# Optimization experiments

Hardware: AMD Instinct MI355X
Metric: run time of the kernel (lower is better)

## Reference

```python
import jax, jax.numpy as jnp
import numpy as np

NEG_INF = -1e9  # additive mask value for masked softmax


def setup_inputs() -> dict:
    key = jax.random.key(0)
    k1, k2, k3, k4, k5 = jax.random.split(key, 5)
    bz, rv_num, rv_len, in_feat, out_feat = 32, 10, 128, 300, 128
    seq_a = jax.random.normal(k1, (bz, rv_num, rv_len, in_feat), dtype=jnp.float32)
    seq_b = jax.random.normal(k2, (bz, rv_num, rv_len, in_feat), dtype=jnp.float32)
    mask_a = jax.random.randint(k3, (bz, rv_num, rv_len), 0, 2, dtype=jnp.int32)
    mask_b = jax.random.randint(k4, (bz, rv_num, rv_len), 0, 2, dtype=jnp.int32)
    # guarantee at least one valid position per review (avoid fully-masked rows)
    mask_a = mask_a.at[:, :, 0].set(1)
    mask_b = mask_b.at[:, :, 0].set(1)
    # FC transform params (xavier-normal-ish weight, zero bias)
    W = jax.random.normal(k5, (in_feat, out_feat), dtype=jnp.float32) * (2.0 / np.sqrt(in_feat + out_feat))
    b = jnp.zeros((out_feat,), dtype=jnp.float32)
    return {"seq_a": seq_a, "seq_b": seq_b, "mask_a": mask_a, "mask_b": mask_b, "W": W, "b": b}


def _masked_softmax(scores, mask):
    # scores: [N, L], mask: [N, L] in {0,1}
    logits = jnp.where(mask > 0, scores, NEG_INF)
    return jax.nn.softmax(logits, axis=-1)


def reference(seq_a, seq_b, mask_a, mask_b, W, b):
    bz, rv_num, rv_len, _ = seq_a.shape
    hdim = W.shape[1]
    N = bz * rv_num          # flattened batch of reviews
    M = rv_num * rv_len      # all tokens on the other side

    # FC + ReLU feature transform
    ta = jax.nn.relu(jnp.einsum('bnld,dh->bnlh', seq_a, W) + b)
    tb = jax.nn.relu(jnp.einsum('bnld,dh->bnlh', seq_b, W) + b)

    sa = ta.reshape(N, rv_len, hdim)
    sb = tb.reshape(N, rv_len, hdim)
    # expand: each review attends over ALL tokens of the other sequence in its sample
    ea = jnp.broadcast_to(ta.reshape(bz, 1, M, hdim), (bz, rv_num, M, hdim)).reshape(N, M, hdim)
    eb = jnp.broadcast_to(tb.reshape(bz, 1, M, hdim), (bz, rv_num, M, hdim)).reshape(N, M, hdim)

    # DOT interaction (no scale): affinity [N, rv_len, M]
    atob_aff = jnp.einsum('nld,nmd->nlm', sa, eb)
    btoa_aff = jnp.einsum('nld,nmd->nlm', sb, ea)

    # MEAN pooling over the other-sequence axis
    atob_scores = atob_aff.mean(axis=-1)  # [N, rv_len]
    btoa_scores = btoa_aff.mean(axis=-1)

    ma = mask_a.reshape(N, rv_len)
    mb = mask_b.reshape(N, rv_len)
    atob_w = _masked_softmax(atob_scores, ma)
    btoa_w = _masked_softmax(btoa_scores, mb)

    a_out = jnp.einsum('nl,nld->nd', atob_w, sa)
    b_out = jnp.einsum('nl,nld->nd', btoa_w, sb)
    return (a_out, b_out, atob_w, btoa_w)
```

## Files before the change

### kernel.cpp

```cpp
#include <hip/hip_runtime.h>
#include <hip/hip_bf16.h>


#define K_FEAT 300
#define H 128
#define NTOK 40960
#define NREV 320
#define TOK_PER_SAMPLE 1280
#define TM 128
#define BLKS_PER_SAMPLE 10
#define LDA 40
#define NCHUNK 10
#define WCHUNK (2 * H * LDA)

typedef __attribute__((ext_vector_type(8))) short bf16x8;
typedef __attribute__((ext_vector_type(4))) float f32x4;
typedef unsigned short u16;
typedef unsigned int u32;

static __device__ __forceinline__ u16 f2bf(float x) {
    u32 u = __float_as_uint(x);
    return (u16)((u + 0x7fffu + ((u >> 16) & 1u)) >> 16);
}
static __device__ __forceinline__ float bf2f(u16 s) {
    return __uint_as_float(((u32)s) << 16);
}

__global__ void wsplit_kernel(const float* __restrict__ W, u16* __restrict__ Wc)
{
    int i = blockIdx.x * 256 + threadIdx.x;
    if (i >= NCHUNK * WCHUNK) return;
    int c = i / WCHUNK;
    int rem = i - c * WCHUNK;
    int part = rem / (H * LDA);
    int rem2 = rem - part * (H * LDA);
    int h = rem2 / LDA;
    int kk = rem2 - h * LDA;
    int k = c * 32 + kk;
    float w = (kk < 32 && k < K_FEAT) ? W[(size_t)k * H + h] : 0.f;
    u16 hi = f2bf(w);
    Wc[i] = part ? f2bf(w - bf2f(hi)) : hi;
}

__global__ __launch_bounds__(256, 3) void fc_mfma_kernel(
    const float* __restrict__ seq_a, const float* __restrict__ seq_b,
    const u16* __restrict__ Wc, const float* __restrict__ bias,
    float* __restrict__ ta, float* __restrict__ tb,
    float* __restrict__ psum_a, float* __restrict__ psum_b)
{
    __shared__ u16 Ah_s[TM * LDA];
    __shared__ u16 Al_s[TM * LDA];
    __shared__ u16 W_s[WCHUNK];
    __shared__ float bias_s[H];

    int blk = blockIdx.x;
    const float* seq; float* outp; float* psum;
    if (blk < 320) { seq = seq_a; outp = ta; psum = psum_a; }
    else           { seq = seq_b; outp = tb; psum = psum_b; blk -= 320; }

    const int tid = threadIdx.x;
    const int tok0 = blk * TM;
    const int wave = tid >> 6;
    const int lane = tid & 63;
    const int nn = lane & 15;
    const int quad = lane >> 4;

    if (tid < H) bias_s[tid] = bias[tid];

    f32x4 acc[8][2];
#pragma unroll
    for (int m = 0; m < 8; ++m) {
        acc[m][0] = (f32x4){0.f, 0.f, 0.f, 0.f};
        acc[m][1] = (f32x4){0.f, 0.f, 0.f, 0.f};
    }

    for (int c = 0; c < NCHUNK; ++c) {
        __syncthreads();
#pragma unroll
        for (int it = 0; it < 4; ++it) {
            int i = tid + it * 256;
            int t = i >> 3;
            int j = i & 7;
            int kk = c * 32 + 4 * j;
            float4 v = make_float4(0.f, 0.f, 0.f, 0.f);
            if (kk + 4 <= K_FEAT)
                v = *(const float4*)&seq[(size_t)(tok0 + t) * K_FEAT + kk];
            u16 h0 = f2bf(v.x), h1 = f2bf(v.y), h2 = f2bf(v.z), h3 = f2bf(v.w);
            uint2 hp, lp;
            hp.x = (u32)h0 | ((u32)h1 << 16);
            hp.y = (u32)h2 | ((u32)h3 << 16);
            lp.x = (u32)f2bf(v.x - bf2f(h0)) | ((u32)f2bf(v.y - bf2f(h1)) << 16);
            lp.y = (u32)f2bf(v.z - bf2f(h2)) | ((u32)f2bf(v.w - bf2f(h3)) << 16);
            *(uint2*)&Ah_s[t * LDA + 4 * j] = hp;
            *(uint2*)&Al_s[t * LDA + 4 * j] = lp;
        }
        const u16* wsrc = Wc + (size_t)c * WCHUNK;
#pragma unroll
        for (int it = 0; it < 5; ++it) {
            int i = tid + it * 256;
            *(uint4*)&W_s[i * 8] = *(const uint4*)&wsrc[i * 8];
        }
        __syncthreads();

        bf16x8 bh0 = *(const bf16x8*)&W_s[((2 * wave + 0) * 16 + nn) * LDA + quad * 8];
        bf16x8 bl0 = *(const bf16x8*)&W_s[5120 + ((2 * wave + 0) * 16 + nn) * LDA + quad * 8];
        bf16x8 bh1 = *(const bf16x8*)&W_s[((2 * wave + 1) * 16 + nn) * LDA + quad * 8];
        bf16x8 bl1 = *(const bf16x8*)&W_s[5120 + ((2 * wave + 1) * 16 + nn) * LDA + quad * 8];
#pragma unroll
        for (int m = 0; m < 8; ++m) {
            bf16x8 a_hi = *(const bf16x8*)&Ah_s[(m * 16 + nn) * LDA + quad * 8];
            bf16x8 a_lo = *(const bf16x8*)&Al_s[(m * 16 + nn) * LDA + quad * 8];
            acc[m][0] = __builtin_amdgcn_mfma_f32_16x16x32_bf16(a_hi, bh0, acc[m][0], 0, 0, 0);
            acc[m][0] = __builtin_amdgcn_mfma_f32_16x16x32_bf16(a_hi, bl0, acc[m][0], 0, 0, 0);
            acc[m][0] = __builtin_amdgcn_mfma_f32_16x16x32_bf16(a_lo, bh0, acc[m][0], 0, 0, 0);
            acc[m][1] = __builtin_amdgcn_mfma_f32_16x16x32_bf16(a_hi, bh1, acc[m][1], 0, 0, 0);
            acc[m][1] = __builtin_amdgcn_mfma_f32_16x16x32_bf16(a_hi, bl1, acc[m][1], 0, 0, 0);
            acc[m][1] = __builtin_amdgcn_mfma_f32_16x16x32_bf16(a_lo, bh1, acc[m][1], 0, 0, 0);
        }
    }

#pragma unroll
    for (int t2 = 0; t2 < 2; ++t2) {
        int hcol = (2 * wave + t2) * 16 + nn;
        float bv = bias_s[hcol];
        float fs = 0.f;
#pragma unroll
        for (int m = 0; m < 8; ++m) {
#pragma unroll
            for (int reg = 0; reg < 4; ++reg) {
                int tok = tok0 + m * 16 + quad * 4 + reg;
                float v = fmaxf(acc[m][t2][reg] + bv, 0.f);
                outp[(size_t)tok * H + hcol] = v;
                fs += v;
            }
        }
        fs += __shfl_xor(fs, 16);
        fs += __shfl_xor(fs, 32);
        if (quad == 0) psum[(size_t)blk * H + hcol] = fs;
    }
}

__global__ __launch_bounds__(256) void attn_kernel(
    const float* __restrict__ ta, const float* __restrict__ tb,
    const int* __restrict__ mask_a, const int* __restrict__ mask_b,
    const float* __restrict__ psum_a, const float* __restrict__ psum_b,
    float* __restrict__ out)
{
    int n = blockIdx.x;
    int side = 0;
    if (n >= NREV) { side = 1; n -= NREV; }

    const float* t = side ? tb : ta;
    const int* mask = side ? mask_b : mask_a;
    const float* psum_o = side ? psum_a : psum_b;
    float* out_vec = out + (side ? NREV * H : 0);
    float* out_w = out + 2 * NREV * H + (side ? NREV * H : 0);

    int sample = n / 10;
    int tid = threadIdx.x;

    __shared__ float score_part[128 * 33];
    __shared__ float mean_s[128];
    __shared__ float w_s[128];
    __shared__ float red[4];
    __shared__ float part_out[8 * 128];

    if (tid < 128) {
        float s = 0.f;
        const float* pb = psum_o + (size_t)sample * BLKS_PER_SAMPLE * H + tid;
#pragma unroll
        for (int i = 0; i < BLKS_PER_SAMPLE; ++i) s += pb[(size_t)i * H];
        mean_s[tid] = s * (1.0f / (float)TOK_PER_SAMPLE);
    }
    __syncthreads();

    const float* rowbase = t + (size_t)n * 128 * H;

#pragma unroll
    for (int i = 0; i < 16; ++i) {
        int q = tid + 256 * i;
        int r = q >> 5;
        int c4 = q & 31;
        float4 v = *(const float4*)&rowbase[q * 4];
        float4 m = *(const float4*)&mean_s[c4 * 4];
        score_part[r * 33 + c4] = v.x * m.x + v.y * m.y + v.z * m.z + v.w * m.w;
    }
    __syncthreads();

    float logit = -1e9f;
    if (tid < 128) {
        float s = 0.f;
#pragma unroll
        for (int j = 0; j < 32; ++j) s += score_part[tid * 33 + j];
        int mv = mask[n * 128 + tid];
        logit = (mv > 0) ? s : -1e9f;
    }

    float mx = logit;
    for (int off = 32; off > 0; off >>= 1) mx = fmaxf(mx, __shfl_xor(mx, off));
    if ((tid & 63) == 0) red[tid >> 6] = mx;
    __syncthreads();
    mx = fmaxf(fmaxf(red[0], red[1]), fmaxf(red[2], red[3]));
    __syncthreads();

    float e = __expf(logit - mx);
    float ssum = e;
    for (int off = 32; off > 0; off >>= 1) ssum += __shfl_xor(ssum, off);
    if ((tid & 63) == 0) red[tid >> 6] = ssum;
    __syncthreads();
    ssum = red[0] + red[1] + red[2] + red[3];

    float w = e / ssum;
    if (tid < 128) {
        w_s[tid] = w;
        out_w[n * 128 + tid] = w;
    }
    __syncthreads();

    int c4 = tid & 31;
    int lp = tid >> 5;
    float4 o4 = make_float4(0.f, 0.f, 0.f, 0.f);
#pragma unroll
    for (int k = 0; k < 16; ++k) {
        int l = k * 8 + lp;
        float wl = w_s[l];
        float4 v = *(const float4*)&rowbase[(size_t)l * H + c4 * 4];
        o4.x = fmaf(wl, v.x, o4.x);
        o4.y = fmaf(wl, v.y, o4.y);
        o4.z = fmaf(wl, v.z, o4.z);
        o4.w = fmaf(wl, v.w, o4.w);
    }
    *(float4*)&part_out[lp * 128 + c4 * 4] = o4;
    __syncthreads();
    if (tid < 128) {
        float o = 0.f;
#pragma unroll
        for (int p = 0; p < 8; ++p) o += part_out[p * 128 + tid];
        out_vec[n * 128 + tid] = o;
    }
}

extern "C" void kernel_launch(void* const* d_in, const int* in_sizes, int n_in,
                              void* d_out, int out_size, void* d_ws, size_t ws_size,
                              hipStream_t stream)
{
    const float* seq_a = (const float*)d_in[0];
    const float* seq_b = (const float*)d_in[1];
    const int* mask_a = (const int*)d_in[2];
    const int* mask_b = (const int*)d_in[3];
    const float* W = (const float*)d_in[4];
    const float* bias = (const float*)d_in[5];
    float* out = (float*)d_out;

    float* ws = (float*)d_ws;
    float* ta = ws;
    float* tb = ta + (size_t)NTOK * H;
    float* psum_a = tb + (size_t)NTOK * H;
    float* psum_b = psum_a + NREV * H;
    u16* Wc = (u16*)(psum_b + NREV * H);

    wsplit_kernel<<<(NCHUNK * WCHUNK + 255) / 256, 256, 0, stream>>>(W, Wc);
    fc_mfma_kernel<<<640, 256, 0, stream>>>(seq_a, seq_b, Wc, bias, ta, tb, psum_a, psum_b);
    attn_kernel<<<640, 256, 0, stream>>>(ta, tb, mask_a, mask_b, psum_a, psum_b, out);
}
```

Baseline: 169.6 us.

## Prefetch next activation chunk into registers and read W fragments directly from global

The FC kernel now loads the next K-chunk of the input sequence into registers while the MFMAs for the current chunk run, then converts it to split bf16 and stores it to shared memory after a barrier. The weight preprocessing is changed to emit a per-wave, per-lane fragment layout, so each wave reads its B operands straight from global/L2 and the shared-memory W tile and its copy are gone. This aims to hide global load latency and cut LDS traffic, at the cost of extra registers and a second barrier per chunk.

```diff
diff --git a/kernel.cpp b/kernel.cpp
--- a/kernel.cpp
+++ b/kernel.cpp
@@ -11,7 +11,7 @@
 #define BLKS_PER_SAMPLE 10
 #define LDA 40
 #define NCHUNK 10
-#define WCHUNK (2 * H * LDA)
+#define WFRAG_ELEMS (NCHUNK * 4 * 4 * 64 * 8)
 
 typedef __attribute__((ext_vector_type(8))) short bf16x8;
 typedef __attribute__((ext_vector_type(4))) float f32x4;
@@ -26,31 +26,32 @@
     return __uint_as_float(((u32)s) << 16);
 }
 
-__global__ void wsplit_kernel(const float* __restrict__ W, u16* __restrict__ Wc)
+__global__ void wsplit_kernel(const float* __restrict__ W, u16* __restrict__ Wfrag)
 {
     int i = blockIdx.x * 256 + threadIdx.x;
-    if (i >= NCHUNK * WCHUNK) return;
-    int c = i / WCHUNK;
-    int rem = i - c * WCHUNK;
-    int part = rem / (H * LDA);
-    int rem2 = rem - part * (H * LDA);
-    int h = rem2 / LDA;
-    int kk = rem2 - h * LDA;
-    int k = c * 32 + kk;
-    float w = (kk < 32 && k < K_FEAT) ? W[(size_t)k * H + h] : 0.f;
+    if (i >= WFRAG_ELEMS) return;
+    int j    = i & 7;
+    int lane = (i >> 3) & 63;
+    int frag = (i >> 9) & 3;
+    int wave = (i >> 11) & 3;
+    int c    = i >> 13;
+    int nn = lane & 15, quad = lane >> 4;
+    int t2 = frag >> 1, part = frag & 1;
+    int h = (2 * wave + t2) * 16 + nn;
+    int k = c * 32 + quad * 8 + j;
+    float w = (k < K_FEAT) ? W[(size_t)k * H + h] : 0.f;
     u16 hi = f2bf(w);
-    Wc[i] = part ? f2bf(w - bf2f(hi)) : hi;
+    Wfrag[i] = part ? f2bf(w - bf2f(hi)) : hi;
 }
 
 __global__ __launch_bounds__(256, 3) void fc_mfma_kernel(
     const float* __restrict__ seq_a, const float* __restrict__ seq_b,
-    const u16* __restrict__ Wc, const float* __restrict__ bias,
+    const u16* __restrict__ Wfrag, const float* __restrict__ bias,
     float* __restrict__ ta, float* __restrict__ tb,
     float* __restrict__ psum_a, float* __restrict__ psum_b)
 {
     __shared__ u16 Ah_s[TM * LDA];
     __shared__ u16 Al_s[TM * LDA];
-    __shared__ u16 W_s[WCHUNK];
     __shared__ float bias_s[H];
 
     int blk = blockIdx.x;
@@ -67,6 +68,9 @@
 
     if (tid < H) bias_s[tid] = bias[tid];
 
+    const int st_t = tid >> 3;
+    const int st_j = tid & 7;
+
     f32x4 acc[8][2];
 #pragma unroll
     for (int m = 0; m < 8; ++m) {
@@ -74,38 +78,46 @@
         acc[m][1] = (f32x4){0.f, 0.f, 0.f, 0.f};
     }
 
+    float4 pf[4];
+#pragma unroll
+    for (int it = 0; it < 4; ++it) {
+        int t = st_t + it * 32;
+        int kk = 4 * st_j;
+        pf[it] = make_float4(0.f, 0.f, 0.f, 0.f);
+        if (kk + 4 <= K_FEAT)
+            pf[it] = *(const float4*)&seq[(size_t)(tok0 + t) * K_FEAT + kk];
+    }
+#pragma unroll
+    for (int it = 0; it < 4; ++it) {
+        int t = st_t + it * 32;
+        float4 v = pf[it];
+        u16 h0 = f2bf(v.x), h1 = f2bf(v.y), h2 = f2bf(v.z), h3 = f2bf(v.w);
+        uint2 hp, lp;
+        hp.x = (u32)h0 | ((u32)h1 << 16);
+        hp.y = (u32)h2 | ((u32)h3 << 16);
+        lp.x = (u32)f2bf(v.x - bf2f(h0)) | ((u32)f2bf(v.y - bf2f(h1)) << 16);
+        lp.y = (u32)f2bf(v.z - bf2f(h2)) | ((u32)f2bf(v.w - bf2f(h3)) << 16);
+        *(uint2*)&Ah_s[t * LDA + 4 * st_j] = hp;
+        *(uint2*)&Al_s[t * LDA + 4 * st_j] = lp;
+    }
+    __syncthreads();
+
     for (int c = 0; c < NCHUNK; ++c) {
-        __syncthreads();
-#pragma unroll
-        for (int it = 0; it < 4; ++it) {
-            int i = tid + it * 256;
-            int t = i >> 3;
-            int j = i & 7;
-            int kk = c * 32 + 4 * j;
-            float4 v = make_float4(0.f, 0.f, 0.f, 0.f);
-            if (kk + 4 <= K_FEAT)
-                v = *(const float4*)&seq[(size_t)(tok0 + t) * K_FEAT + kk];
-            u16 h0 = f2bf(v.x), h1 = f2bf(v.y), h2 = f2bf(v.z), h3 = f2bf(v.w);
-            uint2 hp, lp;
-            hp.x = (u32)h0 | ((u32)h1 << 16);
-            hp.y = (u32)h2 | ((u32)h3 << 16);
-            lp.x = (u32)f2bf(v.x - bf2f(h0)) | ((u32)f2bf(v.y - bf2f(h1)) << 16);
-            lp.y = (u32)f2bf(v.z - bf2f(h2)) | ((u32)f2bf(v.w - bf2f(h3)) << 16);
-            *(uint2*)&Ah_s[t * LDA + 4 * j] = hp;
-            *(uint2*)&Al_s[t * LDA + 4 * j] = lp;
-        }
-        const u16* wsrc = Wc + (size_t)c * WCHUNK;
-#pragma unroll
-        for (int it = 0; it < 5; ++it) {
-            int i = tid + it * 256;
-            *(uint4*)&W_s[i * 8] = *(const uint4*)&wsrc[i * 8];
-        }
-        __syncthreads();
-
-        bf16x8 bh0 = *(const bf16x8*)&W_s[((2 * wave + 0) * 16 + nn) * LDA + quad * 8];
-        bf16x8 bl0 = *(const bf16x8*)&W_s[5120 + ((2 * wave + 0) * 16 + nn) * LDA + quad * 8];
-        bf16x8 bh1 = *(const bf16x8*)&W_s[((2 * wave + 1) * 16 + nn) * LDA + quad * 8];
-        bf16x8 bl1 = *(const bf16x8*)&W_s[5120 + ((2 * wave + 1) * 16 + nn) * LDA + quad * 8];
+        if (c < NCHUNK - 1) {
+#pragma unroll
+            for (int it = 0; it < 4; ++it) {
+                int t = st_t + it * 32;
+                int kk = (c + 1) * 32 + 4 * st_j;
+                pf[it] = make_float4(0.f, 0.f, 0.f, 0.f);
+                if (kk + 4 <= K_FEAT)
+                    pf[it] = *(const float4*)&seq[(size_t)(tok0 + t) * K_FEAT + kk];
+            }
+        }
+        const u16* wf = Wfrag + (size_t)(c * 4 + wave) * 2048;
+        bf16x8 bh0 = *(const bf16x8*)&wf[0 * 512 + lane * 8];
+        bf16x8 bl0 = *(const bf16x8*)&wf[1 * 512 + lane * 8];
+        bf16x8 bh1 = *(const bf16x8*)&wf[2 * 512 + lane * 8];
+        bf16x8 bl1 = *(const bf16x8*)&wf[3 * 512 + lane * 8];
 #pragma unroll
         for (int m = 0; m < 8; ++m) {
             bf16x8 a_hi = *(const bf16x8*)&Ah_s[(m * 16 + nn) * LDA + quad * 8];
@@ -117,6 +129,23 @@
             acc[m][1] = __builtin_amdgcn_mfma_f32_16x16x32_bf16(a_hi, bl1, acc[m][1], 0, 0, 0);
             acc[m][1] = __builtin_amdgcn_mfma_f32_16x16x32_bf16(a_lo, bh1, acc[m][1], 0, 0, 0);
         }
+        __syncthreads();
+        if (c < NCHUNK - 1) {
+#pragma unroll
+            for (int it = 0; it < 4; ++it) {
+                int t = st_t + it * 32;
+                float4 v = pf[it];
+                u16 h0 = f2bf(v.x), h1 = f2bf(v.y), h2 = f2bf(v.z), h3 = f2bf(v.w);
+                uint2 hp, lp;
+                hp.x = (u32)h0 | ((u32)h1 << 16);
+                hp.y = (u32)h2 | ((u32)h3 << 16);
+                lp.x = (u32)f2bf(v.x - bf2f(h0)) | ((u32)f2bf(v.y - bf2f(h1)) << 16);
+                lp.y = (u32)f2bf(v.z - bf2f(h2)) | ((u32)f2bf(v.w - bf2f(h3)) << 16);
+                *(uint2*)&Ah_s[t * LDA + 4 * st_j] = hp;
+                *(uint2*)&Al_s[t * LDA + 4 * st_j] = lp;
+            }
+            __syncthreads();
+        }
     }
 
 #pragma unroll
@@ -257,9 +286,9 @@
     float* tb = ta + (size_t)NTOK * H;
     float* psum_a = tb + (size_t)NTOK * H;
     float* psum_b = psum_a + NREV * H;
-    u16* Wc = (u16*)(psum_b + NREV * H);
-
-    wsplit_kernel<<<(NCHUNK * WCHUNK + 255) / 256, 256, 0, stream>>>(W, Wc);
-    fc_mfma_kernel<<<640, 256, 0, stream>>>(seq_a, seq_b, Wc, bias, ta, tb, psum_a, psum_b);
+    u16* Wfrag = (u16*)(psum_b + NREV * H);
+
+    wsplit_kernel<<<(WFRAG_ELEMS + 255) / 256, 256, 0, stream>>>(W, Wfrag);
+    fc_mfma_kernel<<<640, 256, 0, stream>>>(seq_a, seq_b, Wfrag, bias, ta, tb, psum_a, psum_b);
     attn_kernel<<<640, 256, 0, stream>>>(ta, tb, mask_a, mask_b, psum_a, psum_b, out);
 }
```

After: 163.6 us. 1.04x faster.
